# Kernel tuning notes

Hardware: AMD Instinct MI355X
Metric: run time of the kernel (lower is better)

## Reference

```python
import jax, jax.numpy as jnp
import numpy as np
from jax import lax

B, C, H, W = 32, 512, 32, 32
NH = 8
ER = 4
DK_RATIO = 0.2
EPS_LN = 1e-6


def _layernorm(t, g, b):
    m = t.mean(-1, keepdims=True)
    v = ((t - m) ** 2).mean(-1, keepdims=True)
    return (t - m) / jnp.sqrt(v + EPS_LN) * g + b


def setup_inputs() -> dict:
    key = jax.random.key(0)
    ks = jax.random.split(key, 24)
    s = 0.02
    dh = C // NH
    return {
        "x": jax.random.normal(ks[0], (B, C, H, W), jnp.float32),
        "mask_u": jax.random.uniform(ks[1], (B, NH, dh, dh), jnp.float32),
        "dw_w": jax.random.normal(ks[2], (C, 1, 3, 3), jnp.float32) * s,
        "dw_b": jnp.zeros((C,), jnp.float32),
        "ln1_g": jnp.ones((C,), jnp.float32),
        "ln1_b": jnp.zeros((C,), jnp.float32),
        "qkv_w": jax.random.normal(ks[3], (3 * C, C), jnp.float32) * s,
        "qkv_b": jnp.zeros((3 * C,), jnp.float32),
        "temp": jnp.ones((NH, 1, 1), jnp.float32),
        "proj_w": jax.random.normal(ks[4], (C, C), jnp.float32) * s,
        "proj_b": jnp.zeros((C,), jnp.float32),
        "ct_w": jax.random.normal(ks[5], (C, C, 2, 2), jnp.float32) * s,  # [in,out,kH,kW]
        "ct_b": jnp.zeros((C,), jnp.float32),
        "ln2_g": jnp.ones((C,), jnp.float32),
        "ln2_b": jnp.zeros((C,), jnp.float32),
        "pw1_w": jax.random.normal(ks[6], (ER * C, C), jnp.float32) * s,
        "pw1_b": jnp.zeros((ER * C,), jnp.float32),
        "pw2_w": jax.random.normal(ks[7], (C, ER * C), jnp.float32) * s,
        "pw2_b": jnp.zeros((C,), jnp.float32),
    }


def reference(x, mask_u, dw_w, dw_b, ln1_g, ln1_b, qkv_w, qkv_b, temp,
              proj_w, proj_b, ct_w, ct_b, ln2_g, ln2_b,
              pw1_w, pw1_b, pw2_w, pw2_b):
    inp = x
    b, c, h, w = x.shape
    # depthwise 3x3 conv + residual
    dw = lax.conv_general_dilated(
        x, dw_w, (1, 1), "SAME", feature_group_count=c,
        dimension_numbers=("NCHW", "OIHW", "NCHW")) + dw_b[None, :, None, None]
    x = dw + inp
    # 2x2 avg pool, stride 2
    hp, wp = h // 2, w // 2
    x = x.reshape(b, c, hp, 2, wp, 2).mean(axis=(3, 5))  # [B,C,hp,wp]
    n = hp * wp
    # tokens [B,N,C] -> LN -> qkv
    t = x.reshape(b, c, n).transpose(0, 2, 1)
    t = _layernorm(t, ln1_g, ln1_b)
    qkv = t @ qkv_w.T + qkv_b                       # [B,N,3C]
    dh = c // NH
    qkv = qkv.reshape(b, n, 3, NH, dh).transpose(2, 0, 3, 1, 4)  # [3,B,h,N,d]
    # cosine (XCA-style) attention: transpose to [B,h,d,N], normalize over N
    q = jnp.swapaxes(qkv[0], -2, -1)
    k = jnp.swapaxes(qkv[1], -2, -1)
    v = jnp.swapaxes(qkv[2], -2, -1)
    q = q / jnp.maximum(jnp.linalg.norm(q, axis=-1, keepdims=True), 1e-12)
    k = k / jnp.maximum(jnp.linalg.norm(k, axis=-1, keepdims=True), 1e-12)
    attn = jnp.einsum("bhdn,bhen->bhde", q, k) * temp  # [B,h,d,d]
    attn = attn + (mask_u < DK_RATIO).astype(attn.dtype) * (-1e12)
    attn = jax.nn.softmax(attn, axis=-1)
    out = jnp.einsum("bhde,bhen->bhdn", attn, v)       # [B,h,d,N]
    out = out.transpose(0, 3, 1, 2).reshape(b, n, c)
    t = out @ proj_w.T + proj_b
    t = t + t
    x = t.transpose(0, 2, 1).reshape(b, c, hp, wp)
    # ConvTranspose2d(C,C,2,stride=2): each pixel expands to 2x2 block
    x = jnp.einsum("bchw,copq->bohpwq", x, ct_w).reshape(b, c, 2 * hp, 2 * wp)
    x = x + ct_b[None, :, None, None]
    # MLP in channels-last
    y = x.transpose(0, 2, 3, 1)                        # [B,H,W,C]
    y = _layernorm(y, ln2_g, ln2_b)
    y = jax.nn.gelu(y @ pw1_w.T + pw1_b, approximate=False)
    y = y @ pw2_w.T + pw2_b
    x = y.transpose(0, 3, 1, 2)
    return inp + x
```

## Files before the change

### kernel.cpp

```cpp
#include <hip/hip_runtime.h>
#include <hip/hip_bf16.h>
#include <math.h>

typedef unsigned short ushort;
typedef __attribute__((ext_vector_type(8))) short short8;
typedef __attribute__((ext_vector_type(8))) unsigned short ushort8;
typedef __attribute__((ext_vector_type(4))) unsigned short ushort4v;
typedef __attribute__((ext_vector_type(4))) float f32x4;

__device__ __forceinline__ ushort f2bb(float v) {
    return __builtin_bit_cast(ushort, __float2bfloat16(v));
}
__device__ __forceinline__ float bf2f(ushort u) {
    return __bfloat162float(__builtin_bit_cast(__hip_bfloat16, u));
}
__device__ __forceinline__ void gl2lds16(const ushort* g, ushort* l) {
    __builtin_amdgcn_global_load_lds(
        (const __attribute__((address_space(1))) unsigned int*)g,
        (__attribute__((address_space(3))) unsigned int*)l, 16, 0, 0);
}


__global__ __launch_bounds__(256) void cvtw_k(const float* __restrict__ in,
                                              ushort* __restrict__ out, int n4) {
    int i = blockIdx.x * 256 + threadIdx.x;
    if (i >= n4) return;
    float4 v = ((const float4*)in)[i];
    ushort4v o;
    o.x = f2bb(v.x); o.y = f2bb(v.y); o.z = f2bb(v.z); o.w = f2bb(v.w);
    ((ushort4v*)out)[i] = o;
}

__global__ __launch_bounds__(256) void cvtt_k(const float* __restrict__ in,
                                              ushort* __restrict__ out) {
    __shared__ float tl[32][33];
    int c0 = blockIdx.y * 32, j0 = blockIdx.x * 32;
    int tr = threadIdx.x >> 5, tc = threadIdx.x & 31;
#pragma unroll
    for (int p4 = 0; p4 < 4; ++p4)
        tl[tr + p4 * 8][tc] = in[(size_t)(c0 + tr + p4 * 8) * 2048 + j0 + tc];
    __syncthreads();
#pragma unroll
    for (int p4 = 0; p4 < 4; ++p4)
        out[(size_t)(j0 + tr + p4 * 8) * 512 + c0 + tc] = f2bb(tl[tc][tr + p4 * 8]);
}

__global__ __launch_bounds__(256) void dwpool_k(const float* __restrict__ x,
                                                const float* __restrict__ dww,
                                                const float* __restrict__ dwb,
                                                ushort* __restrict__ xp) {
    int bc = blockIdx.x;
    int c = bc & 511;
    __shared__ float tile[32][33];
    __shared__ float w9[9];
    const float* xb = x + (size_t)bc * 1024;
    int tid = threadIdx.x;
    for (int i = tid; i < 1024; i += 256) tile[i >> 5][i & 31] = xb[i];
    if (tid < 9) w9[tid] = dww[c * 9 + tid];
    __syncthreads();
    float bv = dwb[c];
    int ph = tid >> 4, pw = tid & 15;
    float s = 0.f;
#pragma unroll
    for (int dy = 0; dy < 2; ++dy) {
#pragma unroll
        for (int dx = 0; dx < 2; ++dx) {
            int hh = 2 * ph + dy, ww = 2 * pw + dx;
            float a = bv + tile[hh][ww];
#pragma unroll
            for (int ky = 0; ky < 3; ++ky) {
                int yy = hh + ky - 1;
                if (yy < 0 || yy > 31) continue;
#pragma unroll
                for (int kx = 0; kx < 3; ++kx) {
                    int xx = ww + kx - 1;
                    if (xx < 0 || xx > 31) continue;
                    a += w9[ky * 3 + kx] * tile[yy][xx];
                }
            }
            s += a;
        }
    }
    xp[(size_t)bc * 256 + tid] = f2bb(0.25f * s);
}

__global__ __launch_bounds__(256) void ln1_stats_k(const ushort* __restrict__ xp,
                                                   float* __restrict__ m1,
                                                   float* __restrict__ r1) {
    __shared__ float sh_s[4][64], sh_q[4][64];
    int blk = blockIdx.x;
    int b = blk >> 2;
    int n0 = (blk & 3) * 64;
    int t = threadIdx.x & 63, w = threadIdx.x >> 6;
    float s = 0.f, ss = 0.f;
    for (int i = 0; i < 128; ++i) {
        int c = w * 128 + i;
        float v = bf2f(xp[(size_t)(b * 512 + c) * 256 + n0 + t]);
        s += v; ss += v * v;
    }
    sh_s[w][t] = s; sh_q[w][t] = ss;
    __syncthreads();
    if (w == 0) {
        s  = sh_s[0][t] + sh_s[1][t] + sh_s[2][t] + sh_s[3][t];
        ss = sh_q[0][t] + sh_q[1][t] + sh_q[2][t] + sh_q[3][t];
        float m = s * (1.0f / 512.0f);
        m1[b * 256 + n0 + t] = m;
        r1[b * 256 + n0 + t] = rsqrtf(ss * (1.0f / 512.0f) - m * m + 1e-6f);
    }
}

__global__ __launch_bounds__(256) void ln1_apply_k(const ushort* __restrict__ xp,
                                                   const float* __restrict__ m1,
                                                   const float* __restrict__ r1,
                                                   const float* __restrict__ g,
                                                   const float* __restrict__ beta,
                                                   ushort* __restrict__ a_ln) {
    __shared__ float tl[64][66];
    int blk = blockIdx.x;
    int b = blk >> 5, ct = (blk >> 2) & 7, nt = blk & 3;
    int t = threadIdx.x;
    int rq = t >> 6, nl = t & 63;
#pragma unroll
    for (int i = 0; i < 16; ++i) {
        int r = rq * 16 + i;
        int c = ct * 64 + r;
        tl[r][nl] = bf2f(xp[(size_t)(b * 512 + c) * 256 + nt * 64 + nl]);
    }
    __syncthreads();
    int r2 = t >> 2, cq = t & 3;
    int m = b * 256 + nt * 64 + r2;
    float mu = m1[m], rs = r1[m];
#pragma unroll
    for (int hh = 0; hh < 2; ++hh) {
        ushort8 o;
#pragma unroll
        for (int j = 0; j < 8; ++j) {
            int cl = cq * 16 + hh * 8 + j;
            int c = ct * 64 + cl;
            o[j] = f2bb((tl[cl][r2] - mu) * rs * g[c] + beta[c]);
        }
        *(ushort8*)&a_ln[(size_t)m * 512 + ct * 64 + cq * 16 + hh * 8] = o;
    }
}

__global__ __launch_bounds__(256) void ln2_fuse_k(ushort* __restrict__ yB,
                                                  ushort* __restrict__ yT,
                                                  const float* __restrict__ g,
                                                  const float* __restrict__ beta) {
    int w = threadIdx.x >> 6, lane = threadIdx.x & 63;
    int row = blockIdx.x * 4 + w;
    ushort* base = (row < 8192) ? (yB + (size_t)row * 512)
                                : (yT + (size_t)(row - 8192) * 512);
    ushort8 raw = *(ushort8*)&base[lane * 8];
    float v[8];
    float s = 0.f, ss = 0.f;
#pragma unroll
    for (int j = 0; j < 8; ++j) { v[j] = bf2f(raw[j]); s += v[j]; ss += v[j] * v[j]; }
#pragma unroll
    for (int off = 1; off < 64; off <<= 1) { s += __shfl_xor(s, off); ss += __shfl_xor(ss, off); }
    float mu = s * (1.0f / 512.0f);
    float rs = rsqrtf(ss * (1.0f / 512.0f) - mu * mu + 1e-6f);
    ushort8 o;
#pragma unroll
    for (int j = 0; j < 8; ++j) {
        int c = lane * 8 + j;
        o[j] = f2bb((v[j] - mu) * rs * g[c] + beta[c]);
    }
    *(ushort8*)&base[lane * 8] = o;
}

struct GP {
    const ushort* A;
    const ushort* W;
    const float* bias;
    ushort* outB;
    ushort* outB2;
    float* outF;
    const float* inp;
    int K, m0;
};

template <int MODE, int BN>
__global__ __launch_bounds__(256) void mgemm_k(GP p) {
    constexpr int MT = (BN == 128) ? 4 : 2;
    constexpr int NT = 4;
    constexpr int ATILE = 128 * 32;
    constexpr int BTILE = BN * 32;
    constexpr int SMEM_US = 2 * (ATILE + BTILE);
    __shared__ __align__(16) ushort smem[SMEM_US];
    int tid = threadIdx.x;
    int lane = tid & 63, w = tid >> 6;
    int lr = lane & 15, lq = lane >> 4;
    int mwoff = (BN == 128) ? (w >> 1) * 64 : w * 32;
    int nwoff = (BN == 128) ? (w & 1) * 64 : 0;
    int gx = gridDim.x;
    int wgid = blockIdx.y * gx + blockIdx.x;
    int cpx = (gx * gridDim.y) >> 3;
    int swz = (wgid & 7) * cpx + (wgid >> 3);
    int bx = swz % gx, by = swz / gx;
    int mbase = by * 128, nbase = bx * BN;
    int lsub = lane >> 2;
    int cchunk = (lane & 3) ^ ((lsub >> 1) & 3);
    int lcol = cchunk * 8;
    int physc = lq ^ ((lr >> 1) & 3);
    f32x4 acc[MT][NT] = {};

    auto stage = [&](int buf, int kb) {
        ushort* Ab = smem + buf * ATILE;
        ushort* Bb = smem + 2 * ATILE + buf * BTILE;
#pragma unroll
        for (int i = 0; i < 2; ++i) {
            int row = w * 32 + i * 16;
            gl2lds16(p.A + (size_t)(mbase + row + lsub) * p.K + kb + lcol,
                     &Ab[row * 32]);
        }
        if constexpr (BN == 128) {
#pragma unroll
            for (int i = 0; i < 2; ++i) {
                int row = w * 32 + i * 16;
                gl2lds16(p.W + (size_t)(nbase + row + lsub) * p.K + kb + lcol,
                         &Bb[row * 32]);
            }
        } else {
            int row = w * 16;
            gl2lds16(p.W + (size_t)(nbase + row + lsub) * p.K + kb + lcol,
                     &Bb[row * 32]);
        }
    };

    stage(0, 0);
    __syncthreads();
    int nk = p.K >> 5;
    for (int t = 0; t < nk; ++t) {
        int cur = t & 1;
        if (t + 1 < nk) stage(cur ^ 1, (t + 1) << 5);
        const ushort* Ac = smem + cur * ATILE;
        const ushort* Bc = smem + 2 * ATILE + cur * BTILE;
        short8 af[MT], bfr[NT];
#pragma unroll
        for (int tt = 0; tt < MT; ++tt)
            af[tt] = *(const short8*)&Ac[(mwoff + tt * 16 + lr) * 32 + physc * 8];
#pragma unroll
        for (int tt = 0; tt < NT; ++tt)
            bfr[tt] = *(const short8*)&Bc[(nwoff + tt * 16 + lr) * 32 + physc * 8];
#pragma unroll
        for (int i = 0; i < MT; ++i)
#pragma unroll
            for (int j = 0; j < NT; ++j)
                acc[i][j] = __builtin_amdgcn_mfma_f32_16x16x32_bf16(af[i], bfr[j], acc[i][j], 0, 0, 0);
        __syncthreads();
    }

    if constexpr (MODE == 1 || MODE == 3) {
        const size_t LD = (MODE == 1) ? 512 : 2048;
        ushort* eb = (ushort*)smem;
#pragma unroll
        for (int h = 0; h < 2; ++h) {
            __syncthreads();
            if ((w & 1) == h) {
#pragma unroll
                for (int ti = 0; ti < MT; ++ti)
#pragma unroll
                    for (int tj = 0; tj < NT; ++tj)
#pragma unroll
                        for (int r = 0; r < 4; ++r) {
                            int row = mwoff + ti * 16 + lq * 4 + r;
                            int colh = tj * 16 + lr;
                            float v = acc[ti][tj][r] + p.bias[nbase + h * 64 + colh];
                            if constexpr (MODE == 1) v *= 2.0f;
                            else v = 0.5f * v * (1.0f + erff(v * 0.70710678118654752f));
                            int ph = (colh >> 3) ^ (row & 7);
                            eb[row * 64 + ph * 8 + (colh & 7)] = f2bb(v);
                        }
            }
            __syncthreads();
#pragma unroll
            for (int i = 0; i < 4; ++i) {
                int row = i * 32 + (tid >> 3);
                int ch = tid & 7;
                int pch = ch ^ (row & 7);
                short8 d = *(short8*)&eb[row * 64 + pch * 8];
                *(short8*)&p.outB[(size_t)(mbase + row) * LD + nbase + h * 64 + ch * 8] = d;
            }
        }
    } else if constexpr (MODE == 0) {
        ushort* eb = (ushort*)smem;
        int b = mbase >> 8, n0 = mbase & 255;
#pragma unroll
        for (int pc = 0; pc < 4; ++pc) {
            __syncthreads();
            if ((w & 1) == (pc >> 1)) {
                int tjb = (pc & 1) * 2;
#pragma unroll
                for (int ti = 0; ti < MT; ++ti)
#pragma unroll
                    for (int tj2 = 0; tj2 < 2; ++tj2)
#pragma unroll
                        for (int r = 0; r < 4; ++r) {
                            int tj = tjb + tj2;
                            int row = mwoff + ti * 16 + lq * 4 + r;
                            int cl = tj2 * 16 + lr;
                            float v = acc[ti][tj][r] + p.bias[nbase + pc * 32 + cl];
                            eb[cl * 136 + row] = f2bb(v);
                        }
            }
            __syncthreads();
            if (nbase < 1024) {
#pragma unroll
                for (int i = 0; i < 2; ++i) {
                    int dl = (tid >> 4) + 16 * i;
                    int ch = tid & 15;
                    short8 d = *(short8*)&eb[dl * 136 + ch * 8];
                    int cg = nbase + pc * 32 + dl;
                    int sect = cg >> 9, hh = (cg >> 6) & 7, dd = cg & 63;
                    size_t addr = ((size_t)(sect * 256 + b * 8 + hh) * 64 + dd) * 256 + n0 + ch * 8;
                    *(short8*)&p.outB[addr] = d;
                }
            } else {
                int cv = nbase + pc * 32 - 1024;
                int bh2 = b * 8 + (cv >> 6);
                int d0 = cv & 63;
#pragma unroll
                for (int i = 0; i < 2; ++i) {
                    int idx = i * 256 + tid;
                    int n = idx >> 2, oc = idx & 3;
                    ushort8 dv;
#pragma unroll
                    for (int j = 0; j < 8; ++j) dv[j] = eb[(oc * 8 + j) * 136 + n];
                    *(ushort8*)&p.outB[(size_t)8388608 + (size_t)bh2 * 16384 +
                                       (size_t)(n0 + n) * 64 + d0 + oc * 8] = dv;
                }
            }
        }
    } else if constexpr (MODE == 2) {
        ushort* eb = (ushort*)smem;
        ushort* ybase = (mbase < 2048) ? p.outB : (p.outB2 - (size_t)8192 * 512);
        int obase = nbase >> 2;
#pragma unroll
        for (int hf = 0; hf < 2; ++hf) {
            __syncthreads();
            if ((w >> 1) == hf) {
#pragma unroll
                for (int ti = 0; ti < MT; ++ti)
#pragma unroll
                    for (int tj = 0; tj < NT; ++tj)
#pragma unroll
                        for (int r = 0; r < 4; ++r) {
                            int rl = (mwoff - hf * 64) + ti * 16 + lq * 4 + r;
                            int cgl = nwoff + tj * 16 + lr;
                            int o_l = cgl >> 2, pp = (cgl >> 1) & 1, qq = cgl & 1;
                            int pix = ((rl >> 4) * 2 + pp) * 32 + (rl & 15) * 2 + qq;
                            float v = acc[ti][tj][r] + p.bias[obase + o_l];
                            eb[pix * 40 + o_l] = f2bb(v);
                        }
            }
            __syncthreads();
            int hhbase = ((mbase & 255) >> 4) + hf * 4;
            int prb = (mbase >> 8) * 32 + 2 * hhbase;
#pragma unroll
            for (int i = 0; i < 4; ++i) {
                int pix = i * 64 + (tid >> 2);
                int ch = tid & 3;
                short8 d = *(short8*)&eb[pix * 40 + ch * 8];
                int pr = (prb + (pix >> 5)) * 32 + (pix & 31);
                *(short8*)&ybase[(size_t)pr * 512 + obase + ch * 8] = d;
            }
        }
    } else {
        float* ef = (float*)smem;
        int gm0 = p.m0 + mbase;
        int b = gm0 >> 10, hw0 = gm0 & 1023;
#pragma unroll
        for (int pc = 0; pc < 2; ++pc) {
            __syncthreads();
#pragma unroll
            for (int ti = 0; ti < MT; ++ti)
#pragma unroll
                for (int tj2 = 0; tj2 < 2; ++tj2)
#pragma unroll
                    for (int r = 0; r < 4; ++r) {
                        int tj = pc * 2 + tj2;
                        int row = mwoff + ti * 16 + lq * 4 + r;
                        int cl = tj2 * 16 + lr;
                        ef[cl * 132 + row] = acc[ti][tj][r] + p.bias[nbase + pc * 32 + cl];
                    }
            __syncthreads();
#pragma unroll
            for (int i = 0; i < 4; ++i) {
                int cl = (tid >> 5) + 8 * i;
                int ck = tid & 31;
                float4 v4 = *(float4*)&ef[cl * 132 + ck * 4];
                int c = nbase + pc * 32 + cl;
                size_t idx = ((size_t)(b * 512 + c)) * 1024 + hw0 + ck * 4;
                float4 xin = *(const float4*)&p.inp[idx];
                float4 o4;
                o4.x = xin.x + v4.x; o4.y = xin.y + v4.y;
                o4.z = xin.z + v4.z; o4.w = xin.w + v4.w;
                *(float4*)&p.outF[idx] = o4;
            }
        }
    }
}

__global__ __launch_bounds__(256) void attn_k(const ushort* __restrict__ qkvp,
                                              const float* __restrict__ mask_u,
                                              const float* __restrict__ temp,
                                              ushort* __restrict__ attn_out) {
    __shared__ float Sb[64 * 65];
    __shared__ ushort Pb[64 * 64];
    __shared__ float fq[64], fk[64];
    int tid = threadIdx.x;
    int bh = blockIdx.x;
    int b = bh >> 3, h = bh & 7;
    const ushort* q  = qkvp + (size_t)bh * 16384;
    const ushort* k  = qkvp + 4194304 + (size_t)bh * 16384;
    const ushort* vt = qkvp + 8388608 + (size_t)bh * 16384;
    int lane = tid & 63, w = tid >> 6;
    int lr = lane & 15, lq = lane >> 4;

    {
        int row = tid >> 2, qd = tid & 3;
        const ushort* qr = q + row * 256 + qd * 64;
        const ushort* kr = k + row * 256 + qd * 64;
        float s = 0.f, t = 0.f;
#pragma unroll
        for (int i = 0; i < 8; ++i) {
            short8 a8 = *(const short8*)&qr[i * 8];
            short8 b8 = *(const short8*)&kr[i * 8];
#pragma unroll
            for (int j = 0; j < 8; ++j) {
                float fa = bf2f((ushort)a8[j]); s += fa * fa;
                float fb = bf2f((ushort)b8[j]); t += fb * fb;
            }
        }
        s += __shfl_xor(s, 1); s += __shfl_xor(s, 2);
        t += __shfl_xor(t, 1); t += __shfl_xor(t, 2);
        if (qd == 0) {
            fq[row] = 1.0f / fmaxf(sqrtf(s), 1e-12f);
            fk[row] = 1.0f / fmaxf(sqrtf(t), 1e-12f);
        }
    }
    __syncthreads();

    int mq = (w >> 1) * 32, nq = (w & 1) * 32;
    f32x4 acc[2][2] = {};
    for (int kb = 0; kb < 256; kb += 32) {
        short8 af[2], bfr[2];
#pragma unroll
        for (int ti = 0; ti < 2; ++ti)
            af[ti] = *(const short8*)&q[(mq + ti * 16 + lr) * 256 + kb + lq * 8];
#pragma unroll
        for (int tj = 0; tj < 2; ++tj)
            bfr[tj] = *(const short8*)&k[(nq + tj * 16 + lr) * 256 + kb + lq * 8];
#pragma unroll
        for (int i = 0; i < 2; ++i)
#pragma unroll
            for (int j = 0; j < 2; ++j)
                acc[i][j] = __builtin_amdgcn_mfma_f32_16x16x32_bf16(af[i], bfr[j], acc[i][j], 0, 0, 0);
    }

    float tv = temp[h];
#pragma unroll
    for (int i = 0; i < 2; ++i)
#pragma unroll
        for (int r = 0; r < 4; ++r) {
            int d = mq + i * 16 + lq * 4 + r;
#pragma unroll
            for (int j = 0; j < 2; ++j) {
                int e = nq + j * 16 + lr;
                float sc = acc[i][j][r] * fq[d] * fk[e] * tv;
                float mu = mask_u[((size_t)bh * 64 + d) * 64 + e];
                if (mu < 0.2f) sc -= 1e12f;
                Sb[d * 65 + e] = sc;
            }
        }
    __syncthreads();

    {
        int row = tid >> 2, sub = tid & 3;
        float ev[16];
        float mx = -INFINITY;
#pragma unroll
        for (int i = 0; i < 16; ++i) { float s = Sb[row * 65 + sub * 16 + i]; ev[i] = s; mx = fmaxf(mx, s); }
        mx = fmaxf(mx, __shfl_xor(mx, 1));
        mx = fmaxf(mx, __shfl_xor(mx, 2));
        float sum = 0.f;
#pragma unroll
        for (int i = 0; i < 16; ++i) { ev[i] = expf(ev[i] - mx); sum += ev[i]; }
        sum += __shfl_xor(sum, 1);
        sum += __shfl_xor(sum, 2);
        float inv = 1.0f / sum;
        unsigned int* Pb32 = (unsigned int*)Pb;
#pragma unroll
        for (int kk = 0; kk < 8; ++kk) {
            unsigned int lo = f2bb(ev[2 * kk] * inv);
            unsigned int hi = f2bb(ev[2 * kk + 1] * inv);
            int c8 = sub * 2 + (kk >> 2);
            int ph = c8 ^ (row & 7);
            Pb32[row * 32 + ph * 4 + (kk & 3)] = (hi << 16) | lo;
        }
    }
    __syncthreads();

    int nw = w * 64;
    f32x4 o[4][4] = {};
#pragma unroll
    for (int ks = 0; ks < 2; ++ks) {
        short8 pa[4];
#pragma unroll
        for (int mt = 0; mt < 4; ++mt) {
            int d = mt * 16 + lr;
            int ph = (ks * 4 + lq) ^ (d & 7);
            pa[mt] = *(const short8*)&Pb[d * 64 + ph * 8];
        }
#pragma unroll
        for (int nt = 0; nt < 4; ++nt) {
            short8 vb = *(const short8*)&vt[(size_t)(nw + nt * 16 + lr) * 64 + ks * 32 + lq * 8];
#pragma unroll
            for (int mt = 0; mt < 4; ++mt)
                o[mt][nt] = __builtin_amdgcn_mfma_f32_16x16x32_bf16(pa[mt], vb, o[mt][nt], 0, 0, 0);
        }
    }

#pragma unroll
    for (int mt = 0; mt < 4; ++mt) {
        int d0 = mt * 16 + lq * 4;
#pragma unroll
        for (int nt = 0; nt < 4; ++nt) {
            int n = nw + nt * 16 + lr;
            ushort4v ov;
#pragma unroll
            for (int r = 0; r < 4; ++r) ov[r] = f2bb(o[mt][nt][r]);
            *(ushort4v*)&attn_out[((size_t)(b * 256 + n)) * 512 + h * 64 + d0] = ov;
        }
    }
}

extern "C" void kernel_launch(void* const* d_in, const int* in_sizes, int n_in,
                              void* d_out, int out_size, void* d_ws, size_t ws_size,
                              hipStream_t stream) {
    const float* x      = (const float*)d_in[0];
    const float* mask_u = (const float*)d_in[1];
    const float* dw_w   = (const float*)d_in[2];
    const float* dw_b   = (const float*)d_in[3];
    const float* ln1_g  = (const float*)d_in[4];
    const float* ln1_b  = (const float*)d_in[5];
    const float* qkv_w  = (const float*)d_in[6];
    const float* qkv_b  = (const float*)d_in[7];
    const float* temp   = (const float*)d_in[8];
    const float* proj_w = (const float*)d_in[9];
    const float* proj_b = (const float*)d_in[10];
    const float* ct_w   = (const float*)d_in[11];
    const float* ct_b   = (const float*)d_in[12];
    const float* ln2_g  = (const float*)d_in[13];
    const float* ln2_b  = (const float*)d_in[14];
    const float* pw1_w  = (const float*)d_in[15];
    const float* pw1_b  = (const float*)d_in[16];
    const float* pw2_w  = (const float*)d_in[17];
    const float* pw2_b  = (const float*)d_in[18];

    char* wsb = (char*)d_ws;
    float* mean1 = (float*)wsb;
    float* rstd1 = mean1 + 8192;
    ushort* wq = (ushort*)(wsb + 524288);
    ushort* wp = wq + 786432;
    ushort* wc = wp + 262144;
    ushort* w1 = wc + 1048576;
    ushort* w2 = w1 + 1048576;
    ushort* xp     = (ushort*)(wsb + 8912896);
    ushort* t2     = xp;
    ushort* a_ln   = (ushort*)(wsb + 17301504);
    ushort* yB     = a_ln;
    ushort* qkvp   = (ushort*)(wsb + 25690112);
    ushort* attn_o = (ushort*)(wsb + 50855936);
    ushort* h1c    = qkvp;
    ushort* yT     = (ushort*)(wsb + 59244544);

    cvtw_k<<<768,  256, 0, stream>>>(qkv_w,  wq, 196608);
    cvtw_k<<<256,  256, 0, stream>>>(proj_w, wp, 65536);
    cvtw_k<<<1024, 256, 0, stream>>>(pw1_w,  w1, 262144);
    cvtw_k<<<1024, 256, 0, stream>>>(pw2_w,  w2, 262144);
    cvtt_k<<<dim3(64, 16), 256, 0, stream>>>(ct_w, wc);
    dwpool_k<<<32 * 512, 256, 0, stream>>>(x, dw_w, dw_b, xp);
    ln1_stats_k<<<128, 256, 0, stream>>>(xp, mean1, rstd1);
    ln1_apply_k<<<1024, 256, 0, stream>>>(xp, mean1, rstd1, ln1_g, ln1_b, a_ln);
    {
        GP p{}; p.A = a_ln; p.W = wq; p.bias = qkv_b; p.outB = qkvp; p.K = 512;
        mgemm_k<0, 128><<<dim3(12, 64), 256, 0, stream>>>(p);
    }
    attn_k<<<256, 256, 0, stream>>>(qkvp, mask_u, temp, attn_o);
    {
        GP p{}; p.A = attn_o; p.W = wp; p.bias = proj_b; p.outB = t2; p.K = 512;
        mgemm_k<1, 128><<<dim3(4, 64), 256, 0, stream>>>(p);
    }
    {
        GP p{}; p.A = t2; p.W = wc; p.bias = ct_b;
        p.outB = yB; p.outB2 = yT; p.K = 512;
        mgemm_k<2, 128><<<dim3(16, 64), 256, 0, stream>>>(p);
    }
    ln2_fuse_k<<<8192, 256, 0, stream>>>(yB, yT, ln2_g, ln2_b);
    for (int c = 0; c < 4; ++c) {
        int m0 = c * 8192;
        const ushort* yChunk = (c == 0) ? yB : (yT + (size_t)(m0 - 8192) * 512);
        {
            GP p{}; p.A = yChunk; p.W = w1; p.bias = pw1_b; p.outB = h1c; p.K = 512;
            mgemm_k<3, 128><<<dim3(16, 64), 256, 0, stream>>>(p);
        }
        {
            GP p{}; p.A = h1c; p.W = w2; p.bias = pw2_b;
            p.outF = (float*)d_out; p.inp = x; p.K = 2048; p.m0 = m0;
            mgemm_k<4, 64><<<dim3(8, 64), 256, 0, stream>>>(p);
        }
    }
}
```

Measured before the change: 619.1 us.

## Add 256x256-tile 512-thread MFMA GEMM for the pw1 MLP layer

Replaces the generic 128-tile GEMM for the first MLP projection with a dedicated kernel. It uses 256x256 output tiles computed by 8 waves and double-buffered LDS (128 KB dynamic) loaded with direct global-to-LDS copies. It also adds XOR-swizzled layouts, a grouped block-index swizzle for L2 locality, and a fused bias+GELU epilogue that writes through LDS with coalesced stores. The larger tile raises arithmetic intensity and cuts redundant global loads, at the cost of one block per CU with heavy register use and lower occupancy.

```diff
diff --git a/kernel.cpp b/kernel.cpp
--- a/kernel.cpp
+++ b/kernel.cpp
@@ -402,6 +402,122 @@
     }
 }
 
+__global__ __launch_bounds__(512, 2) void mgemm256_pw1_k(GP p) {
+    extern __shared__ ushort smem[];
+    ushort* Ab = smem;
+    ushort* Bb = smem + 32768;
+    int tid = threadIdx.x;
+    int lane = tid & 63, w = tid >> 6;
+    int lr = lane & 15, lq = lane >> 4;
+    int wr = w >> 2, wc = w & 3;
+    int gx = gridDim.x;
+    int wgid = blockIdx.y * gx + blockIdx.x;
+    int cpx = (gx * gridDim.y) >> 3;
+    int swz = (wgid & 7) * cpx + (wgid >> 3);
+    int bx = swz % gx, by = swz / gx;
+    int mbase = by * 256, nbase = bx * 256;
+    const int K = p.K;
+    int srow0 = w * 32 + (lane >> 2);
+    int schunk = lane & 3;
+    f32x4 acc[8][4] = {};
+
+    auto stageA = [&](int buf, int kh, int kb) {
+        ushort* dst = Ab + buf * 16384 + kh * 8192;
+#pragma unroll
+        for (int i = 0; i < 2; ++i) {
+            int row = srow0 + i * 16;
+            int sc = schunk ^ ((row >> 1) & 3);
+            gl2lds16(p.A + (size_t)(mbase + row) * K + kb + kh * 32 + sc * 8,
+                     &dst[(w * 32 + i * 16) * 32]);
+        }
+    };
+    auto stageB = [&](int buf, int kh, int kb) {
+        ushort* dst = Bb + buf * 16384 + kh * 8192;
+#pragma unroll
+        for (int i = 0; i < 2; ++i) {
+            int row = srow0 + i * 16;
+            int sc = schunk ^ ((row >> 1) & 3);
+            gl2lds16(p.W + (size_t)(nbase + row) * K + kb + kh * 32 + sc * 8,
+                     &dst[(w * 32 + i * 16) * 32]);
+        }
+    };
+
+#define KSTEP256(KH, WN, DOSTAGE)                                             \
+    {                                                                         \
+        asm volatile("s_waitcnt vmcnt(" #WN ")" ::: "memory");                \
+        __builtin_amdgcn_s_barrier();                                         \
+        const ushort* Ak = Ab + cur * 16384 + (KH) * 8192;                    \
+        const ushort* Bk = Bb + cur * 16384 + (KH) * 8192;                    \
+        short8 af[8], bfv[4];                                                 \
+        _Pragma("unroll")                                                     \
+        for (int mt = 0; mt < 8; ++mt) {                                      \
+            int row = wr * 128 + mt * 16 + lr;                                \
+            af[mt] = *(const short8*)&Ak[row * 32 + ((lq ^ ((row >> 1) & 3)) << 3)]; \
+        }                                                                     \
+        _Pragma("unroll")                                                     \
+        for (int nt = 0; nt < 4; ++nt) {                                      \
+            int row = wc * 64 + nt * 16 + lr;                                 \
+            bfv[nt] = *(const short8*)&Bk[row * 32 + ((lq ^ ((row >> 1) & 3)) << 3)]; \
+        }                                                                     \
+        if (DOSTAGE) { stageA(cur ^ 1, KH, kb2); stageB(cur ^ 1, KH, kb2); }  \
+        __builtin_amdgcn_s_setprio(1);                                        \
+        _Pragma("unroll")                                                     \
+        for (int mt = 0; mt < 8; ++mt)                                        \
+            _Pragma("unroll")                                                 \
+            for (int nt = 0; nt < 4; ++nt)                                    \
+                acc[mt][nt] = __builtin_amdgcn_mfma_f32_16x16x32_bf16(        \
+                    af[mt], bfv[nt], acc[mt][nt], 0, 0, 0);                   \
+        __builtin_amdgcn_s_setprio(0);                                        \
+    }
+
+    stageA(0, 0, 0); stageB(0, 0, 0);
+    stageA(0, 1, 0); stageB(0, 1, 0);
+    int T = K >> 6;
+    int t = 0;
+#pragma unroll 1
+    for (; t < T - 1; ++t) {
+        int cur = t & 1;
+        int kb2 = (t + 1) << 6;
+        KSTEP256(0, 4, 1)
+        KSTEP256(1, 4, 1)
+    }
+    {
+        int cur = t & 1;
+        int kb2 = 0; (void)kb2;
+        KSTEP256(0, 4, 0)
+        KSTEP256(1, 0, 0)
+    }
+#undef KSTEP256
+
+    ushort* eb = smem;
+#pragma unroll
+    for (int hf = 0; hf < 2; ++hf) {
+        __syncthreads();
+        if (wr == hf) {
+#pragma unroll
+            for (int mt = 0; mt < 8; ++mt)
+#pragma unroll
+                for (int nt = 0; nt < 4; ++nt)
+#pragma unroll
+                    for (int r = 0; r < 4; ++r) {
+                        int rl = mt * 16 + lq * 4 + r;
+                        int cl = wc * 64 + nt * 16 + lr;
+                        float v = acc[mt][nt][r] + p.bias[nbase + cl];
+                        v = 0.5f * v * (1.0f + erff(v * 0.70710678118654752f));
+                        eb[rl * 256 + (((cl >> 3) ^ (rl & 7)) << 3) + (cl & 7)] = f2bb(v);
+                    }
+        }
+        __syncthreads();
+#pragma unroll
+        for (int i = 0; i < 8; ++i) {
+            int row = (tid >> 5) + i * 16;
+            int ch = tid & 31;
+            short8 d = *(short8*)&eb[row * 256 + ((ch ^ (row & 7)) << 3)];
+            *(short8*)&p.outB[(size_t)(mbase + hf * 128 + row) * 2048 + nbase + ch * 8] = d;
+        }
+    }
+}
+
 __global__ __launch_bounds__(256) void attn_k(const ushort* __restrict__ qkvp,
                                               const float* __restrict__ mask_u,
                                               const float* __restrict__ temp,
@@ -576,6 +692,9 @@
     ushort* h1c    = qkvp;
     ushort* yT     = (ushort*)(wsb + 59244544);
 
+    hipFuncSetAttribute((const void*)mgemm256_pw1_k,
+                        hipFuncAttributeMaxDynamicSharedMemorySize, 131072);
+
     cvtw_k<<<768,  256, 0, stream>>>(qkv_w,  wq, 196608);
     cvtw_k<<<256,  256, 0, stream>>>(proj_w, wp, 65536);
     cvtw_k<<<1024, 256, 0, stream>>>(pw1_w,  w1, 262144);
@@ -604,7 +723,7 @@
         const ushort* yChunk = (c == 0) ? yB : (yT + (size_t)(m0 - 8192) * 512);
         {
             GP p{}; p.A = yChunk; p.W = w1; p.bias = pw1_b; p.outB = h1c; p.K = 512;
-            mgemm_k<3, 128><<<dim3(16, 64), 256, 0, stream>>>(p);
+            mgemm256_pw1_k<<<dim3(8, 32), 512, 131072, stream>>>(p);
         }
         {
             GP p{}; p.A = h1c; p.W = w2; p.bias = pw2_b;
```

Measured after the change: 613.6 us. About the same (-0.9%).

## Fuse MLP pw1+GELU+pw2 into one kernel keeping hidden activations in LDS

Applied to the files above, without the earlier changes.

Replaces the four-chunk loop of two GEMM launches with a single kernel. Each block takes 64 token rows and computes the 2048-wide hidden layer in 256-column slices. Each slice gets GELU applied, is stored as bf16 in LDS, and is immediately consumed by the second GEMM, with the residual added in the epilogue. This removes the global write and read-back of the large hidden activation and cuts kernel launches. In exchange, weights are read straight from global/L2 by every block without LDS staging, so total weight traffic is much higher. The 96KB LDS footprint also limits occupancy to one block per CU.

```diff
diff --git a/kernel.cpp b/kernel.cpp
--- a/kernel.cpp
+++ b/kernel.cpp
@@ -366,38 +366,105 @@
                 *(short8*)&ybase[(size_t)pr * 512 + obase + ch * 8] = d;
             }
         }
-    } else {
-        float* ef = (float*)smem;
-        int gm0 = p.m0 + mbase;
-        int b = gm0 >> 10, hw0 = gm0 & 1023;
-#pragma unroll
-        for (int pc = 0; pc < 2; ++pc) {
-            __syncthreads();
-#pragma unroll
-            for (int ti = 0; ti < MT; ++ti)
-#pragma unroll
-                for (int tj2 = 0; tj2 < 2; ++tj2)
-#pragma unroll
-                    for (int r = 0; r < 4; ++r) {
-                        int tj = pc * 2 + tj2;
-                        int row = mwoff + ti * 16 + lq * 4 + r;
-                        int cl = tj2 * 16 + lr;
-                        ef[cl * 132 + row] = acc[ti][tj][r] + p.bias[nbase + pc * 32 + cl];
-                    }
-            __syncthreads();
-#pragma unroll
-            for (int i = 0; i < 4; ++i) {
-                int cl = (tid >> 5) + 8 * i;
-                int ck = tid & 31;
-                float4 v4 = *(float4*)&ef[cl * 132 + ck * 4];
-                int c = nbase + pc * 32 + cl;
-                size_t idx = ((size_t)(b * 512 + c)) * 1024 + hw0 + ck * 4;
-                float4 xin = *(const float4*)&p.inp[idx];
-                float4 o4;
-                o4.x = xin.x + v4.x; o4.y = xin.y + v4.y;
-                o4.z = xin.z + v4.z; o4.w = xin.w + v4.w;
-                *(float4*)&p.outF[idx] = o4;
-            }
+    }
+}
+
+__global__ __launch_bounds__(512) void mlp_fused_k(
+    const ushort* __restrict__ yB, const ushort* __restrict__ yT,
+    const ushort* __restrict__ w1, const ushort* __restrict__ w2,
+    const float* __restrict__ b1, const float* __restrict__ b2,
+    const float* __restrict__ inp, float* __restrict__ outF) {
+    __shared__ __align__(16) ushort Asm[64 * 512];
+    __shared__ __align__(16) ushort Hsm[64 * 256];
+    int tid = threadIdx.x;
+    int lane = tid & 63, w = tid >> 6;
+    int lr = lane & 15, lq = lane >> 4;
+    int wgid = blockIdx.x;
+    int swz = (wgid & 7) * 64 + (wgid >> 3);
+    int mbase = swz * 64;
+    const ushort* yb = (mbase < 8192) ? (yB + (size_t)mbase * 512)
+                                      : (yT + (size_t)(mbase - 8192) * 512);
+#pragma unroll
+    for (int j = 0; j < 8; ++j) {
+        int row = w * 8 + j;
+        int sc = lane ^ (row & 7);
+        gl2lds16(yb + (size_t)row * 512 + sc * 8, &Asm[row * 512]);
+    }
+    int ocol0 = w * 64;
+    int hcol0 = w * 32;
+    float b2v[4];
+#pragma unroll
+    for (int nt = 0; nt < 4; ++nt) b2v[nt] = b2[ocol0 + nt * 16 + lr];
+    asm volatile("s_waitcnt vmcnt(0)" ::: "memory");
+    __syncthreads();
+
+    f32x4 acc2[4][4] = {};
+#pragma unroll 1
+    for (int hb = 0; hb < 8; ++hb) {
+        f32x4 acc1[4][2] = {};
+#pragma unroll
+        for (int kh = 0; kh < 16; ++kh) {
+            short8 bf1[2];
+#pragma unroll
+            for (int nt = 0; nt < 2; ++nt)
+                bf1[nt] = *(const short8*)&w1[(size_t)(hb * 256 + hcol0 + nt * 16 + lr) * 512 + kh * 32 + lq * 8];
+#pragma unroll
+            for (int mt = 0; mt < 4; ++mt) {
+                int row = mt * 16 + lr;
+                int c = kh * 4 + lq;
+                short8 af = *(const short8*)&Asm[row * 512 + ((c ^ (row & 7)) << 3)];
+#pragma unroll
+                for (int nt = 0; nt < 2; ++nt)
+                    acc1[mt][nt] = __builtin_amdgcn_mfma_f32_16x16x32_bf16(af, bf1[nt], acc1[mt][nt], 0, 0, 0);
+            }
+        }
+        __syncthreads();
+#pragma unroll
+        for (int mt = 0; mt < 4; ++mt)
+#pragma unroll
+            for (int nt = 0; nt < 2; ++nt)
+#pragma unroll
+                for (int r = 0; r < 4; ++r) {
+                    int row = mt * 16 + lq * 4 + r;
+                    int hl = hcol0 + nt * 16 + lr;
+                    float v = acc1[mt][nt][r] + b1[hb * 256 + hl];
+                    v = 0.5f * v * (1.0f + erff(v * 0.70710678118654752f));
+                    int c = hl >> 3;
+                    Hsm[row * 256 + ((c ^ (row & 7)) << 3) + (hl & 7)] = f2bb(v);
+                }
+        __syncthreads();
+#pragma unroll
+        for (int kh = 0; kh < 8; ++kh) {
+            short8 bf2[4];
+#pragma unroll
+            for (int nt = 0; nt < 4; ++nt)
+                bf2[nt] = *(const short8*)&w2[(size_t)(ocol0 + nt * 16 + lr) * 2048 + hb * 256 + kh * 32 + lq * 8];
+#pragma unroll
+            for (int mt = 0; mt < 4; ++mt) {
+                int row = mt * 16 + lr;
+                int c = kh * 4 + lq;
+                short8 ha = *(const short8*)&Hsm[row * 256 + ((c ^ (row & 7)) << 3)];
+#pragma unroll
+                for (int nt = 0; nt < 4; ++nt)
+                    acc2[mt][nt] = __builtin_amdgcn_mfma_f32_16x16x32_bf16(ha, bf2[nt], acc2[mt][nt], 0, 0, 0);
+            }
+        }
+    }
+    int b = mbase >> 10;
+    int hwb = mbase & 1023;
+#pragma unroll
+    for (int mt = 0; mt < 4; ++mt) {
+#pragma unroll
+        for (int nt = 0; nt < 4; ++nt) {
+            int col = ocol0 + nt * 16 + lr;
+            size_t idx = ((size_t)(b * 512 + col)) * 1024 + hwb + mt * 16 + lq * 4;
+            float4 xin = *(const float4*)&inp[idx];
+            float4 o4;
+            o4.x = xin.x + acc2[mt][nt][0] + b2v[nt];
+            o4.y = xin.y + acc2[mt][nt][1] + b2v[nt];
+            o4.z = xin.z + acc2[mt][nt][2] + b2v[nt];
+            o4.w = xin.w + acc2[mt][nt][3] + b2v[nt];
+            *(float4*)&outF[idx] = o4;
         }
     }
 }
@@ -573,7 +640,6 @@
     ushort* yB     = a_ln;
     ushort* qkvp   = (ushort*)(wsb + 25690112);
     ushort* attn_o = (ushort*)(wsb + 50855936);
-    ushort* h1c    = qkvp;
     ushort* yT     = (ushort*)(wsb + 59244544);
 
     cvtw_k<<<768,  256, 0, stream>>>(qkv_w,  wq, 196608);
@@ -599,17 +665,6 @@
         mgemm_k<2, 128><<<dim3(16, 64), 256, 0, stream>>>(p);
     }
     ln2_fuse_k<<<8192, 256, 0, stream>>>(yB, yT, ln2_g, ln2_b);
-    for (int c = 0; c < 4; ++c) {
-        int m0 = c * 8192;
-        const ushort* yChunk = (c == 0) ? yB : (yT + (size_t)(m0 - 8192) * 512);
-        {
-            GP p{}; p.A = yChunk; p.W = w1; p.bias = pw1_b; p.outB = h1c; p.K = 512;
-            mgemm_k<3, 128><<<dim3(16, 64), 256, 0, stream>>>(p);
-        }
-        {
-            GP p{}; p.A = h1c; p.W = w2; p.bias = pw2_b;
-            p.outF = (float*)d_out; p.inp = x; p.K = 2048; p.m0 = m0;
-            mgemm_k<4, 64><<<dim3(8, 64), 256, 0, stream>>>(p);
-        }
-    }
-}
+    mlp_fused_k<<<512, 512, 0, stream>>>(yB, yT, w1, w2, pw1_b, pw2_b,
+                                         x, (float*)d_out);
+}
```

Measured after the change: 589.6 us. 1.05x faster.
